# Performance work log

Hardware: AMD Instinct MI355X
Metric: run time of the kernel (lower is better)

## Reference

```python
import jax, jax.numpy as jnp
import numpy as np

NUM_LEVELS = 16
FEATS_PER_LEVEL = 2
LOG2_HASHMAP = 19
TABLE_SIZE = 1 << LOG2_HASHMAP
BASE_RES = 16
DESIRED_RES = 4096
PER_LEVEL_SCALE = float(np.exp(np.log(DESIRED_RES / BASE_RES) / (NUM_LEVELS - 1)))
PRIMES = (np.uint32(1), np.uint32(2654435761), np.uint32(805459861))
N_POINTS = 2_000_000


def _level_features(x, table, level):
    # x: [N,3] in [0,1]; table: [TABLE_SIZE, F]
    scale = BASE_RES * (PER_LEVEL_SCALE ** level) - 1.0
    res = int(np.ceil(scale)) + 1
    dense = (res ** 3) <= TABLE_SIZE  # tcnn uses dense indexing when grid fits
    pos = x * scale + 0.5
    pos0 = jnp.floor(pos)
    w = pos - pos0                     # trilinear weights, [N,3]
    base = pos0.astype(jnp.uint32)
    out = jnp.zeros((x.shape[0], table.shape[1]), dtype=table.dtype)
    for c in range(8):                 # 8 corners of the voxel
        offs = [(c >> d) & 1 for d in range(3)]
        pc = [jnp.minimum(base[:, d] + np.uint32(offs[d]), np.uint32(res - 1)) for d in range(3)]
        if dense:
            idx = pc[0] + pc[1] * np.uint32(res) + pc[2] * np.uint32(res * res)
        else:
            idx = (pc[0] * PRIMES[0]) ^ (pc[1] * PRIMES[1]) ^ (pc[2] * PRIMES[2])
            idx = idx & np.uint32(TABLE_SIZE - 1)
        wt = jnp.ones(x.shape[0], dtype=x.dtype)
        for d in range(3):
            wt = wt * (w[:, d] if offs[d] else (1.0 - w[:, d]))
        out = out + wt[:, None] * table[idx.astype(jnp.int32)]
    return out


def hashgrid_encode(x, tables):
    # x: [N,3] in [0,1]; tables: [L, TABLE_SIZE, F] -> [N, L*F]
    return jnp.concatenate(
        [_level_features(x, tables[l], l) for l in range(NUM_LEVELS)], axis=-1)


def setup_inputs() -> dict:
    key = jax.random.key(0)
    k1, k2, k3, k4, k5 = jax.random.split(key, 5)
    points = jax.random.uniform(k1, (N_POINTS, 3), dtype=jnp.float32)
    # tcnn hashgrid init: uniform(-1e-4, 1e-4)
    tables = jax.random.uniform(k2, (NUM_LEVELS, TABLE_SIZE, FEATS_PER_LEVEL),
                                minval=-1e-4, maxval=1e-4, dtype=jnp.float32)
    def kaiming(k, fan_out, fan_in):
        bound = np.sqrt(2.0) * np.sqrt(3.0 / fan_in)
        return jax.random.uniform(k, (fan_out, fan_in), minval=-bound, maxval=bound,
                                  dtype=jnp.float32)
    W1 = kaiming(k3, 32, 32)
    W2 = kaiming(k4, 32, 32)
    W3 = kaiming(k5, 4, 32)
    aabb = jnp.stack([jnp.zeros(3, jnp.float32), jnp.ones(3, jnp.float32)])
    return {"points": points, "tables": tables, "W1": W1, "W2": W2, "W3": W3,
            "aabb": aabb}


def reference(points, tables, W1, W2, W3, aabb):
    texc = jnp.clip((points - aabb[0][None, :]) / (aabb[1] - aabb[0])[None, :], 0.0, 1.0)
    enc = hashgrid_encode(texc, tables)            # [N, 32]
    h = jax.nn.relu(enc @ W1.T)
    h = jax.nn.relu(h @ W2.T)
    out = h @ W3.T                                 # [N, 4]
    mn = jnp.array([0.0, 0.0, 0.0, 0.01], dtype=out.dtype)
    mx = jnp.array([1.0, 1.0, 1.0, 1.0], dtype=out.dtype)
    return jax.nn.sigmoid(out) * (mx - mn) + mn
```

## Files before the change

kernel.cpp:

```cpp
#include <hip/hip_runtime.h>
#include <cmath>


namespace {
constexpr int kLevels = 16;
constexpr unsigned kTableSize = 1u << 19;
constexpr unsigned kMask = kTableSize - 1u;
constexpr int kCells = 262144;
constexpr int kScanBlocks = 256;

typedef _Float16 half2_t __attribute__((ext_vector_type(2)));
typedef unsigned int u32;

struct LevelParams {
  float scale[kLevels];
  unsigned res[kLevels];
  int dense[kLevels];
  unsigned toff[kLevels];
  unsigned cnt[kLevels];
};
}

__global__ __launch_bounds__(256)
void conv_tables_kernel(const float2* __restrict__ src, u32* __restrict__ dst,
                        LevelParams lp,
                        const float* __restrict__ W1, const float* __restrict__ W2,
                        const float* __restrict__ W3, half2_t* __restrict__ Wh,
                        u32* __restrict__ hist0)
{
  int gid = blockIdx.x * blockDim.x + threadIdx.x;
  if (gid < 512) {
    Wh[gid] = half2_t{(_Float16)W1[2 * gid], (_Float16)W1[2 * gid + 1]};
  } else if (gid < 1024) {
    int t = gid - 512;
    Wh[512 + t] = half2_t{(_Float16)W2[2 * t], (_Float16)W2[2 * t + 1]};
  } else if (gid < 1088) {
    int t = gid - 1024;
    Wh[1024 + t] = half2_t{(_Float16)W3[2 * t], (_Float16)W3[2 * t + 1]};
  }
  if (hist0 && gid < kCells) hist0[gid] = 0u;
  int l = blockIdx.x >> 11;
  unsigned e = (unsigned)((blockIdx.x & 2047) * blockDim.x + threadIdx.x);
  if (l < kLevels && e < lp.cnt[l]) {
    float2 v = src[(size_t)l * kTableSize + e];
    dst[lp.toff[l] + e] =
        __builtin_bit_cast(u32, half2_t{(_Float16)v.x, (_Float16)v.y});
  }
}

__device__ __forceinline__ void texc_of(const float* __restrict__ pts,
                                        const float* __restrict__ aabb, int i,
                                        float& x, float& y, float& z)
{
  float a0x = aabb[0], a0y = aabb[1], a0z = aabb[2];
  float a1x = aabb[3], a1y = aabb[4], a1z = aabb[5];
  x = fminf(fmaxf((pts[3 * i + 0] - a0x) / (a1x - a0x), 0.f), 1.f);
  y = fminf(fmaxf((pts[3 * i + 1] - a0y) / (a1y - a0y), 0.f), 1.f);
  z = fminf(fmaxf((pts[3 * i + 2] - a0z) / (a1z - a0z), 0.f), 1.f);
}

__device__ __forceinline__ int cell_of(float x, float y, float z)
{
  int cx = min((int)(x * 64.f), 63);
  int cy = min((int)(y * 64.f), 63);
  int cz = min((int)(z * 64.f), 63);
  return cx + (cy << 6) + (cz << 12);
}

__global__ __launch_bounds__(256)
void hist_kernel(const float* __restrict__ points, const float* __restrict__ aabb,
                 u32* __restrict__ hist, int n)
{
  int i = blockIdx.x * blockDim.x + threadIdx.x;
  if (i >= n) return;
  float x, y, z;
  texc_of(points, aabb, i, x, y, z);
  atomicAdd(&hist[cell_of(x, y, z)], 1u);
}

__global__ __launch_bounds__(1024)
void scanA_kernel(u32* __restrict__ hist, u32* __restrict__ btot)
{
  __shared__ u32 sm[1024];
  int t = threadIdx.x;
  int i = (blockIdx.x << 10) + t;
  u32 x = hist[i];
  sm[t] = x;
  __syncthreads();
  u32 v = x;
  for (int off = 1; off < 1024; off <<= 1) {
    u32 a = (t >= off) ? sm[t - off] : 0u;
    __syncthreads();
    v += a;
    sm[t] = v;
    __syncthreads();
  }
  hist[i] = v - x;
  if (t == 1023) btot[blockIdx.x] = v;
}

__global__ __launch_bounds__(256)
void scanB_kernel(const u32* __restrict__ btot, u32* __restrict__ bbase)
{
  __shared__ u32 sm[256];
  int t = threadIdx.x;
  u32 x = btot[t];
  sm[t] = x;
  __syncthreads();
  u32 v = x;
  for (int off = 1; off < 256; off <<= 1) {
    u32 a = (t >= off) ? sm[t - off] : 0u;
    __syncthreads();
    v += a;
    sm[t] = v;
    __syncthreads();
  }
  bbase[t] = v - x;
}

__global__ __launch_bounds__(256)
void scatter_kernel(const float* __restrict__ points, const float* __restrict__ aabb,
                    u32* __restrict__ hist, const u32* __restrict__ bbase,
                    float4* __restrict__ sorted, u32* __restrict__ perm, int n)
{
  int i = blockIdx.x * blockDim.x + threadIdx.x;
  if (i >= n) return;
  float x, y, z;
  texc_of(points, aabb, i, x, y, z);
  int c = cell_of(x, y, z);
  u32 slot = bbase[c >> 10] + atomicAdd(&hist[c], 1u);
  sorted[slot] = float4{x, y, z, 0.f};
  perm[slot] = (u32)i;
}

__device__ __forceinline__ u32 sel4(uint4 v, u32 j) {
  u32 lo = (j & 1u) ? v.y : v.x;
  u32 hi = (j & 1u) ? v.w : v.z;
  return (j & 2u) ? hi : lo;
}

__global__ __launch_bounds__(256)
void encode_kernel(const float4* __restrict__ pts,
                   const u32* __restrict__ tables,
                   half2_t* __restrict__ enc,
                   LevelParams lp, int n, int bpl)
{
  int l = blockIdx.x / bpl;
  int i = (blockIdx.x - l * bpl) * blockDim.x + threadIdx.x;
  if (i >= n) return;

  float4 p = pts[i];
  float x = p.x, y = p.y, z = p.z;

  float s = lp.scale[l];
  unsigned res = lp.res[l];
  bool dense = (lp.dense[l] != 0);
  unsigned rm1 = res - 1u;
  unsigned res2 = res * res;
  const u32* tab = tables + lp.toff[l];

  float fx = x * s + 0.5f, fy = y * s + 0.5f, fz = z * s + 0.5f;
  float fx0 = floorf(fx), fy0 = floorf(fy), fz0 = floorf(fz);
  float wx = fx - fx0, wy = fy - fy0, wz = fz - fz0;
  unsigned bx = (unsigned)fx0, by = (unsigned)fy0, bz = (unsigned)fz0;

  unsigned pcx0 = min(bx, rm1), pcx1 = min(bx + 1u, rm1);

  u32 idx0[4], idx1[4];
  #pragma unroll
  for (int q = 0; q < 4; ++q) {
    unsigned oy = (unsigned)(q & 1);
    unsigned oz = (unsigned)(q >> 1);
    unsigned pcy = min(by + oy, rm1);
    unsigned pcz = min(bz + oz, rm1);
    if (dense) {
      u32 b = pcy * res + pcz * res2;
      idx0[q] = pcx0 + b;
      idx1[q] = pcx1 + b;
    } else {
      u32 h = (pcy * 2654435761u) ^ (pcz * 805459861u);
      idx0[q] = (pcx0 ^ h) & kMask;
      idx1[q] = (pcx1 ^ h) & kMask;
    }
  }

  uint4 v[4];
  #pragma unroll
  for (int q = 0; q < 4; ++q)
    v[q] = *reinterpret_cast<const uint4*>(tab + (idx0[q] & ~3u));

  u32 e1x[4] = {0u, 0u, 0u, 0u};
  #pragma unroll
  for (int q = 0; q < 4; ++q) {
    if ((idx0[q] ^ idx1[q]) >= 4u) e1x[q] = tab[idx1[q]];
  }

  float wx1 = wx, wx0 = 1.f - wx;
  float acc0 = 0.f, acc1 = 0.f;
  #pragma unroll
  for (int q = 0; q < 4; ++q) {
    unsigned oy = (unsigned)(q & 1);
    unsigned oz = (unsigned)(q >> 1);
    float wyz = (oy ? wy : 1.f - wy) * (oz ? wz : 1.f - wz);
    u32 e0 = sel4(v[q], idx0[q] & 3u);
    u32 e1g = sel4(v[q], idx1[q] & 3u);
    u32 e1 = ((idx0[q] ^ idx1[q]) < 4u) ? e1g : e1x[q];
    half2_t f0 = __builtin_bit_cast(half2_t, e0);
    half2_t f1 = __builtin_bit_cast(half2_t, e1);
    float w0 = wyz * wx0, w1 = wyz * wx1;
    acc0 += w0 * (float)f0.x + w1 * (float)f1.x;
    acc1 += w0 * (float)f0.y + w1 * (float)f1.y;
  }
  enc[(size_t)l * n + i] = half2_t{(_Float16)acc0, (_Float16)acc1};
}

__global__ __launch_bounds__(256)
void encode_raw_kernel(const float* __restrict__ points,
                       const u32* __restrict__ tables,
                       const float* __restrict__ aabb,
                       half2_t* __restrict__ enc,
                       LevelParams lp, int n, int bpl)
{
  int l = blockIdx.x / bpl;
  int i = (blockIdx.x - l * bpl) * blockDim.x + threadIdx.x;
  if (i >= n) return;
  float x, y, z;
  texc_of(points, aabb, i, x, y, z);

  float s = lp.scale[l];
  unsigned res = lp.res[l];
  bool dense = (lp.dense[l] != 0);
  unsigned rm1 = res - 1u;
  unsigned res2 = res * res;
  const u32* tab = tables + lp.toff[l];

  float fx = x * s + 0.5f, fy = y * s + 0.5f, fz = z * s + 0.5f;
  float fx0 = floorf(fx), fy0 = floorf(fy), fz0 = floorf(fz);
  float wx = fx - fx0, wy = fy - fy0, wz = fz - fz0;
  unsigned bx = (unsigned)fx0, by = (unsigned)fy0, bz = (unsigned)fz0;
  unsigned pcx0 = min(bx, rm1), pcx1 = min(bx + 1u, rm1);

  u32 idx0[4], idx1[4];
  #pragma unroll
  for (int q = 0; q < 4; ++q) {
    unsigned oy = (unsigned)(q & 1);
    unsigned oz = (unsigned)(q >> 1);
    unsigned pcy = min(by + oy, rm1);
    unsigned pcz = min(bz + oz, rm1);
    if (dense) {
      u32 b = pcy * res + pcz * res2;
      idx0[q] = pcx0 + b;
      idx1[q] = pcx1 + b;
    } else {
      u32 h = (pcy * 2654435761u) ^ (pcz * 805459861u);
      idx0[q] = (pcx0 ^ h) & kMask;
      idx1[q] = (pcx1 ^ h) & kMask;
    }
  }
  uint4 v[4];
  #pragma unroll
  for (int q = 0; q < 4; ++q)
    v[q] = *reinterpret_cast<const uint4*>(tab + (idx0[q] & ~3u));
  u32 e1x[4] = {0u, 0u, 0u, 0u};
  #pragma unroll
  for (int q = 0; q < 4; ++q) {
    if ((idx0[q] ^ idx1[q]) >= 4u) e1x[q] = tab[idx1[q]];
  }
  float wx1 = wx, wx0 = 1.f - wx;
  float acc0 = 0.f, acc1 = 0.f;
  #pragma unroll
  for (int q = 0; q < 4; ++q) {
    unsigned oy = (unsigned)(q & 1);
    unsigned oz = (unsigned)(q >> 1);
    float wyz = (oy ? wy : 1.f - wy) * (oz ? wz : 1.f - wz);
    u32 e0 = sel4(v[q], idx0[q] & 3u);
    u32 e1g = sel4(v[q], idx1[q] & 3u);
    u32 e1 = ((idx0[q] ^ idx1[q]) < 4u) ? e1g : e1x[q];
    half2_t f0 = __builtin_bit_cast(half2_t, e0);
    half2_t f1 = __builtin_bit_cast(half2_t, e1);
    float w0 = wyz * wx0, w1 = wyz * wx1;
    acc0 += w0 * (float)f0.x + w1 * (float)f1.x;
    acc1 += w0 * (float)f0.y + w1 * (float)f1.y;
  }
  enc[(size_t)l * n + i] = half2_t{(_Float16)acc0, (_Float16)acc1};
}

__device__ __forceinline__ float dot2_acc(half2_t a, half2_t b, float c) {
#if __has_builtin(__builtin_amdgcn_fdot2)
  return __builtin_amdgcn_fdot2(a, b, c, false);
#else
  return c + (float)a.x * (float)b.x + (float)a.y * (float)b.y;
#endif
}

__global__ __launch_bounds__(256)
void mlp_kernel(const half2_t* __restrict__ enc,
                const half2_t* __restrict__ Wh,
                const u32* __restrict__ perm,
                float* __restrict__ out, int n)
{
  int i = blockIdx.x * blockDim.x + threadIdx.x;
  if (i >= n) return;

  u32 orig = perm ? perm[i] : (u32)i;

  half2_t e[16];
  #pragma unroll
  for (int l = 0; l < kLevels; ++l) e[l] = enc[(size_t)l * n + i];

  const half2_t* W1h = Wh;
  const half2_t* W2h = Wh + 512;
  const half2_t* W3h = Wh + 1024;

  float h1f[32];
  #pragma unroll
  for (int j = 0; j < 32; ++j) {
    float acc = 0.f;
    #pragma unroll
    for (int k = 0; k < 16; ++k) acc = dot2_acc(e[k], W1h[16 * j + k], acc);
    h1f[j] = fmaxf(acc, 0.f);
  }
  half2_t h1[16];
  #pragma unroll
  for (int k = 0; k < 16; ++k)
    h1[k] = half2_t{(_Float16)h1f[2 * k], (_Float16)h1f[2 * k + 1]};

  float h2f[32];
  #pragma unroll
  for (int j = 0; j < 32; ++j) {
    float acc = 0.f;
    #pragma unroll
    for (int k = 0; k < 16; ++k) acc = dot2_acc(h1[k], W2h[16 * j + k], acc);
    h2f[j] = fmaxf(acc, 0.f);
  }
  half2_t h2[16];
  #pragma unroll
  for (int k = 0; k < 16; ++k)
    h2[k] = half2_t{(_Float16)h2f[2 * k], (_Float16)h2f[2 * k + 1]};

  float o[4];
  #pragma unroll
  for (int j = 0; j < 4; ++j) {
    float acc = 0.f;
    #pragma unroll
    for (int k = 0; k < 16; ++k) acc = dot2_acc(h2[k], W3h[16 * j + k], acc);
    o[j] = acc;
  }

  float4 r;
  r.x = 1.f / (1.f + __expf(-o[0]));
  r.y = 1.f / (1.f + __expf(-o[1]));
  r.z = 1.f / (1.f + __expf(-o[2]));
  r.w = 0.99f / (1.f + __expf(-o[3])) + 0.01f;
  reinterpret_cast<float4*>(out)[orig] = r;
}

__global__ __launch_bounds__(256)
void hashgrid_mlp_kernel(const float* __restrict__ points,
                         const float* __restrict__ tables,
                         const float* __restrict__ W1,
                         const float* __restrict__ W2,
                         const float* __restrict__ W3,
                         const float* __restrict__ aabb,
                         float* __restrict__ out,
                         LevelParams lp, int n)
{
  int i = blockIdx.x * blockDim.x + threadIdx.x;
  if (i >= n) return;
  float x, y, z;
  texc_of(points, aabb, i, x, y, z);
  float enc[2 * kLevels];
  #pragma unroll
  for (int l = 0; l < kLevels; ++l) {
    float s = lp.scale[l];
    unsigned res = lp.res[l];
    bool dense = (lp.dense[l] != 0);
    unsigned rm1 = res - 1u;
    unsigned res2 = res * res;
    float fx = x * s + 0.5f, fy = y * s + 0.5f, fz = z * s + 0.5f;
    float fx0 = floorf(fx), fy0 = floorf(fy), fz0 = floorf(fz);
    float wx = fx - fx0, wy = fy - fy0, wz = fz - fz0;
    unsigned bx = (unsigned)fx0, by = (unsigned)fy0, bz = (unsigned)fz0;
    const float2* tab = reinterpret_cast<const float2*>(tables) + (size_t)l * kTableSize;
    float acc0 = 0.f, acc1 = 0.f;
    #pragma unroll
    for (int c = 0; c < 8; ++c) {
      unsigned ox = (unsigned)(c & 1);
      unsigned oy = (unsigned)((c >> 1) & 1);
      unsigned oz = (unsigned)((c >> 2) & 1);
      unsigned pcx = min(bx + ox, rm1);
      unsigned pcy = min(by + oy, rm1);
      unsigned pcz = min(bz + oz, rm1);
      unsigned idx;
      if (dense) idx = pcx + pcy * res + pcz * res2;
      else idx = (pcx ^ (pcy * 2654435761u) ^ (pcz * 805459861u)) & kMask;
      float wt = (ox ? wx : 1.f - wx) * (oy ? wy : 1.f - wy) * (oz ? wz : 1.f - wz);
      float2 f = tab[idx];
      acc0 += wt * f.x;
      acc1 += wt * f.y;
    }
    enc[2 * l + 0] = acc0;
    enc[2 * l + 1] = acc1;
  }
  float h1[32];
  #pragma unroll
  for (int j = 0; j < 32; ++j) {
    float acc = 0.f;
    #pragma unroll
    for (int k = 0; k < 32; ++k) acc += enc[k] * W1[32 * j + k];
    h1[j] = fmaxf(acc, 0.f);
  }
  float h2[32];
  #pragma unroll
  for (int j = 0; j < 32; ++j) {
    float acc = 0.f;
    #pragma unroll
    for (int k = 0; k < 32; ++k) acc += h1[k] * W2[32 * j + k];
    h2[j] = fmaxf(acc, 0.f);
  }
  float o[4];
  #pragma unroll
  for (int j = 0; j < 4; ++j) {
    float acc = 0.f;
    #pragma unroll
    for (int k = 0; k < 32; ++k) acc += h2[k] * W3[32 * j + k];
    o[j] = acc;
  }
  float4 r;
  r.x = 1.f / (1.f + __expf(-o[0]));
  r.y = 1.f / (1.f + __expf(-o[1]));
  r.z = 1.f / (1.f + __expf(-o[2]));
  r.w = 0.99f / (1.f + __expf(-o[3])) + 0.01f;
  reinterpret_cast<float4*>(out)[i] = r;
}

extern "C" void kernel_launch(void* const* d_in, const int* in_sizes, int n_in,
                              void* d_out, int out_size, void* d_ws, size_t ws_size,
                              hipStream_t stream) {
  const float* points = (const float*)d_in[0];
  const float* tables = (const float*)d_in[1];
  const float* W1     = (const float*)d_in[2];
  const float* W2     = (const float*)d_in[3];
  const float* W3     = (const float*)d_in[4];
  const float* aabb   = (const float*)d_in[5];
  float* out = (float*)d_out;
  int n = in_sizes[0] / 3;

  LevelParams lp;
  const double pls = std::exp(std::log(4096.0 / 16.0) / 15.0);
  unsigned off = 0;
  for (int l = 0; l < kLevels; ++l) {
    double s = 16.0 * std::pow(pls, (double)l) - 1.0;
    lp.scale[l] = (float)s;
    long long res = (long long)std::ceil(s) + 1;
    lp.res[l] = (unsigned)res;
    long long r3 = res * res * res;
    lp.dense[l] = (r3 <= (long long)kTableSize) ? 1 : 0;
    lp.cnt[l] = lp.dense[l] ? (unsigned)r3 : kTableSize;
    lp.toff[l] = off;
    off += (lp.cnt[l] + 3u) & ~3u;
  }

  const int block = 256;
  const size_t tab_f16_bytes = (size_t)off * sizeof(u32);
  const size_t enc_bytes     = (size_t)kLevels * (size_t)n * sizeof(half2_t);
  const size_t perm_bytes    = (size_t)n * sizeof(u32);
  const size_t w_bytes       = 1088 * sizeof(half2_t);

  const size_t need_sorted = tab_f16_bytes + enc_bytes + perm_bytes + w_bytes;
  const size_t need_raw    = tab_f16_bytes + enc_bytes + w_bytes;
  const bool out_fits_sorted = (size_t)out_size >= (size_t)4 * (size_t)n;
  const bool enc_fits_hist = enc_bytes >= (size_t)(kCells + 512) * sizeof(u32);

  const int grid_n = (n + block - 1) / block;
  const int bpl = grid_n;

  if (ws_size >= need_sorted && out_fits_sorted && enc_fits_hist) {
    char* p = (char*)d_ws;
    u32*     tab_f16 = (u32*)p;                   p += tab_f16_bytes;
    half2_t* enc     = (half2_t*)p;               p += enc_bytes;
    u32*     perm    = (u32*)p;                   p += perm_bytes;
    half2_t* Wh      = (half2_t*)p;
    u32*     hist    = (u32*)enc;
    u32*     btot    = hist + kCells;
    u32*     bbase   = btot + kScanBlocks;
    float4*  sorted  = (float4*)d_out;

    conv_tables_kernel<<<kLevels * 2048, block, 0, stream>>>(
        reinterpret_cast<const float2*>(tables), tab_f16, lp, W1, W2, W3, Wh, hist);
    hist_kernel<<<grid_n, block, 0, stream>>>(points, aabb, hist, n);
    scanA_kernel<<<kScanBlocks, 1024, 0, stream>>>(hist, btot);
    scanB_kernel<<<1, 256, 0, stream>>>(btot, bbase);
    scatter_kernel<<<grid_n, block, 0, stream>>>(points, aabb, hist, bbase,
                                                 sorted, perm, n);
    encode_kernel<<<bpl * kLevels, block, 0, stream>>>(
        sorted, tab_f16, enc, lp, n, bpl);
    mlp_kernel<<<grid_n, block, 0, stream>>>(enc, Wh, perm, out, n);
  } else if (ws_size >= need_raw) {
    char* p = (char*)d_ws;
    u32*     tab_f16 = (u32*)p;                   p += tab_f16_bytes;
    half2_t* enc     = (half2_t*)p;               p += enc_bytes;
    half2_t* Wh      = (half2_t*)p;

    conv_tables_kernel<<<kLevels * 2048, block, 0, stream>>>(
        reinterpret_cast<const float2*>(tables), tab_f16, lp, W1, W2, W3, Wh,
        nullptr);
    encode_raw_kernel<<<bpl * kLevels, block, 0, stream>>>(
        points, tab_f16, aabb, enc, lp, n, bpl);
    mlp_kernel<<<grid_n, block, 0, stream>>>(enc, Wh, nullptr, out, n);
  } else {
    hashgrid_mlp_kernel<<<grid_n, block, 0, stream>>>(
        points, tables, W1, W2, W3, aabb, out, lp, n);
  }
}
```

Baseline: 799.7 us.

## Fuse per-level encode and MLP into one kernel on sorted points

Replaces the separate level-parallel encode kernel and MLP kernel on the sorted path with a single kernel that computes all 16 levels per point and runs the MLP in registers. This removes the intermediate fp16 encoding buffer write and read. The sorted points, perm and histogram now live in workspace instead of aliasing the output and encoding buffers. In exchange, each thread keeps all level lookups and MLP state in registers, so register pressure rises and occupancy may drop. Table locality also changes, since levels are no longer processed one at a time across the grid.

```diff
diff --git a/kernel.cpp b/kernel.cpp
--- a/kernel.cpp
+++ b/kernel.cpp
@@ -139,18 +139,152 @@
   return (j & 2u) ? hi : lo;
 }
 
-__global__ __launch_bounds__(256)
-void encode_kernel(const float4* __restrict__ pts,
-                   const u32* __restrict__ tables,
-                   half2_t* __restrict__ enc,
-                   LevelParams lp, int n, int bpl)
+__device__ __forceinline__ float dot2_acc(half2_t a, half2_t b, float c) {
+#if __has_builtin(__builtin_amdgcn_fdot2)
+  return __builtin_amdgcn_fdot2(a, b, c, false);
+#else
+  return c + (float)a.x * (float)b.x + (float)a.y * (float)b.y;
+#endif
+}
+
+__global__ __launch_bounds__(256)
+void fused_kernel(const float4* __restrict__ pts,
+                  const u32* __restrict__ tables,
+                  const half2_t* __restrict__ Wh,
+                  const u32* __restrict__ perm,
+                  float* __restrict__ out,
+                  LevelParams lp, int n)
+{
+  int i = blockIdx.x * blockDim.x + threadIdx.x;
+  if (i >= n) return;
+
+  u32 orig = perm[i];
+  float4 p = pts[i];
+  float x = p.x, y = p.y, z = p.z;
+
+  half2_t e[kLevels];
+  #pragma unroll
+  for (int l = 0; l < kLevels; ++l) {
+    float s = lp.scale[l];
+    unsigned res = lp.res[l];
+    bool dense = (lp.dense[l] != 0);
+    unsigned rm1 = res - 1u;
+    unsigned res2 = res * res;
+    const u32* tab = tables + lp.toff[l];
+
+    float fx = x * s + 0.5f, fy = y * s + 0.5f, fz = z * s + 0.5f;
+    float fx0 = floorf(fx), fy0 = floorf(fy), fz0 = floorf(fz);
+    float wx = fx - fx0, wy = fy - fy0, wz = fz - fz0;
+    unsigned bx = (unsigned)fx0, by = (unsigned)fy0, bz = (unsigned)fz0;
+    unsigned pcx0 = min(bx, rm1), pcx1 = min(bx + 1u, rm1);
+
+    u32 idx0[4], idx1[4];
+    #pragma unroll
+    for (int q = 0; q < 4; ++q) {
+      unsigned oy = (unsigned)(q & 1);
+      unsigned oz = (unsigned)(q >> 1);
+      unsigned pcy = min(by + oy, rm1);
+      unsigned pcz = min(bz + oz, rm1);
+      if (dense) {
+        u32 b = pcy * res + pcz * res2;
+        idx0[q] = pcx0 + b;
+        idx1[q] = pcx1 + b;
+      } else {
+        u32 h = (pcy * 2654435761u) ^ (pcz * 805459861u);
+        idx0[q] = (pcx0 ^ h) & kMask;
+        idx1[q] = (pcx1 ^ h) & kMask;
+      }
+    }
+
+    uint4 v[4];
+    #pragma unroll
+    for (int q = 0; q < 4; ++q)
+      v[q] = *reinterpret_cast<const uint4*>(tab + (idx0[q] & ~3u));
+
+    u32 e1x[4] = {0u, 0u, 0u, 0u};
+    #pragma unroll
+    for (int q = 0; q < 4; ++q) {
+      if ((idx0[q] ^ idx1[q]) >= 4u) e1x[q] = tab[idx1[q]];
+    }
+
+    float wx1 = wx, wx0 = 1.f - wx;
+    float acc0 = 0.f, acc1 = 0.f;
+    #pragma unroll
+    for (int q = 0; q < 4; ++q) {
+      unsigned oy = (unsigned)(q & 1);
+      unsigned oz = (unsigned)(q >> 1);
+      float wyz = (oy ? wy : 1.f - wy) * (oz ? wz : 1.f - wz);
+      u32 e0 = sel4(v[q], idx0[q] & 3u);
+      u32 e1g = sel4(v[q], idx1[q] & 3u);
+      u32 e1 = ((idx0[q] ^ idx1[q]) < 4u) ? e1g : e1x[q];
+      half2_t f0 = __builtin_bit_cast(half2_t, e0);
+      half2_t f1 = __builtin_bit_cast(half2_t, e1);
+      float w0 = wyz * wx0, w1 = wyz * wx1;
+      acc0 += w0 * (float)f0.x + w1 * (float)f1.x;
+      acc1 += w0 * (float)f0.y + w1 * (float)f1.y;
+    }
+    e[l] = half2_t{(_Float16)acc0, (_Float16)acc1};
+  }
+
+  const half2_t* W1h = Wh;
+  const half2_t* W2h = Wh + 512;
+  const half2_t* W3h = Wh + 1024;
+
+  float h1f[32];
+  #pragma unroll
+  for (int j = 0; j < 32; ++j) {
+    float acc = 0.f;
+    #pragma unroll
+    for (int k = 0; k < 16; ++k) acc = dot2_acc(e[k], W1h[16 * j + k], acc);
+    h1f[j] = fmaxf(acc, 0.f);
+  }
+  half2_t h1[16];
+  #pragma unroll
+  for (int k = 0; k < 16; ++k)
+    h1[k] = half2_t{(_Float16)h1f[2 * k], (_Float16)h1f[2 * k + 1]};
+
+  float h2f[32];
+  #pragma unroll
+  for (int j = 0; j < 32; ++j) {
+    float acc = 0.f;
+    #pragma unroll
+    for (int k = 0; k < 16; ++k) acc = dot2_acc(h1[k], W2h[16 * j + k], acc);
+    h2f[j] = fmaxf(acc, 0.f);
+  }
+  half2_t h2[16];
+  #pragma unroll
+  for (int k = 0; k < 16; ++k)
+    h2[k] = half2_t{(_Float16)h2f[2 * k], (_Float16)h2f[2 * k + 1]};
+
+  float o[4];
+  #pragma unroll
+  for (int j = 0; j < 4; ++j) {
+    float acc = 0.f;
+    #pragma unroll
+    for (int k = 0; k < 16; ++k) acc = dot2_acc(h2[k], W3h[16 * j + k], acc);
+    o[j] = acc;
+  }
+
+  float4 r;
+  r.x = 1.f / (1.f + __expf(-o[0]));
+  r.y = 1.f / (1.f + __expf(-o[1]));
+  r.z = 1.f / (1.f + __expf(-o[2]));
+  r.w = 0.99f / (1.f + __expf(-o[3])) + 0.01f;
+  reinterpret_cast<float4*>(out)[orig] = r;
+}
+
+__global__ __launch_bounds__(256)
+void encode_raw_kernel(const float* __restrict__ points,
+                       const u32* __restrict__ tables,
+                       const float* __restrict__ aabb,
+                       half2_t* __restrict__ enc,
+                       LevelParams lp, int n, int bpl)
 {
   int l = blockIdx.x / bpl;
   int i = (blockIdx.x - l * bpl) * blockDim.x + threadIdx.x;
   if (i >= n) return;
-
-  float4 p = pts[i];
-  float x = p.x, y = p.y, z = p.z;
+  float x, y, z;
+  texc_of(points, aabb, i, x, y, z);
 
   float s = lp.scale[l];
   unsigned res = lp.res[l];
@@ -163,7 +297,6 @@
   float fx0 = floorf(fx), fy0 = floorf(fy), fz0 = floorf(fz);
   float wx = fx - fx0, wy = fy - fy0, wz = fz - fz0;
   unsigned bx = (unsigned)fx0, by = (unsigned)fy0, bz = (unsigned)fz0;
-
   unsigned pcx0 = min(bx, rm1), pcx1 = min(bx + 1u, rm1);
 
   u32 idx0[4], idx1[4];
@@ -183,18 +316,15 @@
       idx1[q] = (pcx1 ^ h) & kMask;
     }
   }
-
   uint4 v[4];
   #pragma unroll
   for (int q = 0; q < 4; ++q)
     v[q] = *reinterpret_cast<const uint4*>(tab + (idx0[q] & ~3u));
-
   u32 e1x[4] = {0u, 0u, 0u, 0u};
   #pragma unroll
   for (int q = 0; q < 4; ++q) {
     if ((idx0[q] ^ idx1[q]) >= 4u) e1x[q] = tab[idx1[q]];
   }
-
   float wx1 = wx, wx0 = 1.f - wx;
   float acc0 = 0.f, acc1 = 0.f;
   #pragma unroll
@@ -215,94 +345,12 @@
 }
 
 __global__ __launch_bounds__(256)
-void encode_raw_kernel(const float* __restrict__ points,
-                       const u32* __restrict__ tables,
-                       const float* __restrict__ aabb,
-                       half2_t* __restrict__ enc,
-                       LevelParams lp, int n, int bpl)
-{
-  int l = blockIdx.x / bpl;
-  int i = (blockIdx.x - l * bpl) * blockDim.x + threadIdx.x;
-  if (i >= n) return;
-  float x, y, z;
-  texc_of(points, aabb, i, x, y, z);
-
-  float s = lp.scale[l];
-  unsigned res = lp.res[l];
-  bool dense = (lp.dense[l] != 0);
-  unsigned rm1 = res - 1u;
-  unsigned res2 = res * res;
-  const u32* tab = tables + lp.toff[l];
-
-  float fx = x * s + 0.5f, fy = y * s + 0.5f, fz = z * s + 0.5f;
-  float fx0 = floorf(fx), fy0 = floorf(fy), fz0 = floorf(fz);
-  float wx = fx - fx0, wy = fy - fy0, wz = fz - fz0;
-  unsigned bx = (unsigned)fx0, by = (unsigned)fy0, bz = (unsigned)fz0;
-  unsigned pcx0 = min(bx, rm1), pcx1 = min(bx + 1u, rm1);
-
-  u32 idx0[4], idx1[4];
-  #pragma unroll
-  for (int q = 0; q < 4; ++q) {
-    unsigned oy = (unsigned)(q & 1);
-    unsigned oz = (unsigned)(q >> 1);
-    unsigned pcy = min(by + oy, rm1);
-    unsigned pcz = min(bz + oz, rm1);
-    if (dense) {
-      u32 b = pcy * res + pcz * res2;
-      idx0[q] = pcx0 + b;
-      idx1[q] = pcx1 + b;
-    } else {
-      u32 h = (pcy * 2654435761u) ^ (pcz * 805459861u);
-      idx0[q] = (pcx0 ^ h) & kMask;
-      idx1[q] = (pcx1 ^ h) & kMask;
-    }
-  }
-  uint4 v[4];
-  #pragma unroll
-  for (int q = 0; q < 4; ++q)
-    v[q] = *reinterpret_cast<const uint4*>(tab + (idx0[q] & ~3u));
-  u32 e1x[4] = {0u, 0u, 0u, 0u};
-  #pragma unroll
-  for (int q = 0; q < 4; ++q) {
-    if ((idx0[q] ^ idx1[q]) >= 4u) e1x[q] = tab[idx1[q]];
-  }
-  float wx1 = wx, wx0 = 1.f - wx;
-  float acc0 = 0.f, acc1 = 0.f;
-  #pragma unroll
-  for (int q = 0; q < 4; ++q) {
-    unsigned oy = (unsigned)(q & 1);
-    unsigned oz = (unsigned)(q >> 1);
-    float wyz = (oy ? wy : 1.f - wy) * (oz ? wz : 1.f - wz);
-    u32 e0 = sel4(v[q], idx0[q] & 3u);
-    u32 e1g = sel4(v[q], idx1[q] & 3u);
-    u32 e1 = ((idx0[q] ^ idx1[q]) < 4u) ? e1g : e1x[q];
-    half2_t f0 = __builtin_bit_cast(half2_t, e0);
-    half2_t f1 = __builtin_bit_cast(half2_t, e1);
-    float w0 = wyz * wx0, w1 = wyz * wx1;
-    acc0 += w0 * (float)f0.x + w1 * (float)f1.x;
-    acc1 += w0 * (float)f0.y + w1 * (float)f1.y;
-  }
-  enc[(size_t)l * n + i] = half2_t{(_Float16)acc0, (_Float16)acc1};
-}
-
-__device__ __forceinline__ float dot2_acc(half2_t a, half2_t b, float c) {
-#if __has_builtin(__builtin_amdgcn_fdot2)
-  return __builtin_amdgcn_fdot2(a, b, c, false);
-#else
-  return c + (float)a.x * (float)b.x + (float)a.y * (float)b.y;
-#endif
-}
-
-__global__ __launch_bounds__(256)
 void mlp_kernel(const half2_t* __restrict__ enc,
                 const half2_t* __restrict__ Wh,
-                const u32* __restrict__ perm,
                 float* __restrict__ out, int n)
 {
   int i = blockIdx.x * blockDim.x + threadIdx.x;
   if (i >= n) return;
-
-  u32 orig = perm ? perm[i] : (u32)i;
 
   half2_t e[16];
   #pragma unroll
@@ -352,7 +400,7 @@
   r.y = 1.f / (1.f + __expf(-o[1]));
   r.z = 1.f / (1.f + __expf(-o[2]));
   r.w = 0.99f / (1.f + __expf(-o[3])) + 0.01f;
-  reinterpret_cast<float4*>(out)[orig] = r;
+  reinterpret_cast<float4*>(out)[i] = r;
 }
 
 __global__ __launch_bounds__(256)
@@ -463,28 +511,26 @@
 
   const int block = 256;
   const size_t tab_f16_bytes = (size_t)off * sizeof(u32);
+  const size_t sorted_bytes  = (size_t)n * sizeof(float4);
+  const size_t perm_bytes    = (size_t)n * sizeof(u32);
+  const size_t hist_bytes    = (size_t)(kCells + 2 * kScanBlocks) * sizeof(u32);
   const size_t enc_bytes     = (size_t)kLevels * (size_t)n * sizeof(half2_t);
-  const size_t perm_bytes    = (size_t)n * sizeof(u32);
   const size_t w_bytes       = 1088 * sizeof(half2_t);
 
-  const size_t need_sorted = tab_f16_bytes + enc_bytes + perm_bytes + w_bytes;
+  const size_t need_sorted = tab_f16_bytes + sorted_bytes + perm_bytes + hist_bytes + w_bytes;
   const size_t need_raw    = tab_f16_bytes + enc_bytes + w_bytes;
-  const bool out_fits_sorted = (size_t)out_size >= (size_t)4 * (size_t)n;
-  const bool enc_fits_hist = enc_bytes >= (size_t)(kCells + 512) * sizeof(u32);
 
   const int grid_n = (n + block - 1) / block;
-  const int bpl = grid_n;
-
-  if (ws_size >= need_sorted && out_fits_sorted && enc_fits_hist) {
+
+  if (ws_size >= need_sorted) {
     char* p = (char*)d_ws;
     u32*     tab_f16 = (u32*)p;                   p += tab_f16_bytes;
-    half2_t* enc     = (half2_t*)p;               p += enc_bytes;
+    float4*  sorted  = (float4*)p;                p += sorted_bytes;
     u32*     perm    = (u32*)p;                   p += perm_bytes;
+    u32*     hist    = (u32*)p;                   p += hist_bytes;
     half2_t* Wh      = (half2_t*)p;
-    u32*     hist    = (u32*)enc;
     u32*     btot    = hist + kCells;
     u32*     bbase   = btot + kScanBlocks;
-    float4*  sorted  = (float4*)d_out;
 
     conv_tables_kernel<<<kLevels * 2048, block, 0, stream>>>(
         reinterpret_cast<const float2*>(tables), tab_f16, lp, W1, W2, W3, Wh, hist);
@@ -493,21 +539,21 @@
     scanB_kernel<<<1, 256, 0, stream>>>(btot, bbase);
     scatter_kernel<<<grid_n, block, 0, stream>>>(points, aabb, hist, bbase,
                                                  sorted, perm, n);
-    encode_kernel<<<bpl * kLevels, block, 0, stream>>>(
-        sorted, tab_f16, enc, lp, n, bpl);
-    mlp_kernel<<<grid_n, block, 0, stream>>>(enc, Wh, perm, out, n);
+    fused_kernel<<<grid_n, block, 0, stream>>>(sorted, tab_f16, Wh, perm, out,
+                                               lp, n);
   } else if (ws_size >= need_raw) {
     char* p = (char*)d_ws;
     u32*     tab_f16 = (u32*)p;                   p += tab_f16_bytes;
     half2_t* enc     = (half2_t*)p;               p += enc_bytes;
     half2_t* Wh      = (half2_t*)p;
 
+    const int bpl = grid_n;
     conv_tables_kernel<<<kLevels * 2048, block, 0, stream>>>(
         reinterpret_cast<const float2*>(tables), tab_f16, lp, W1, W2, W3, Wh,
         nullptr);
     encode_raw_kernel<<<bpl * kLevels, block, 0, stream>>>(
         points, tab_f16, aabb, enc, lp, n, bpl);
-    mlp_kernel<<<grid_n, block, 0, stream>>>(enc, Wh, nullptr, out, n);
+    mlp_kernel<<<grid_n, block, 0, stream>>>(enc, Wh, out, n);
   } else {
     hashgrid_mlp_kernel<<<grid_n, block, 0, stream>>>(
         points, tables, W1, W2, W3, aabb, out, lp, n);
```

Result: slower. 1.495 ms (+87.0%).

## Morton-order cell sort, fold scanB into scatter, pack perm into sorted points

Applied to the files above, without the earlier changes.

Replaces linear cell indexing with a Morton (Z-order) code so sorted points have better 3D locality for table gathers. Removes the separate single-block scan kernel by having each scatter block redo the 256-entry block-total scan in shared memory. Stores the original index in the w lane of the sorted float4, dropping the perm buffer, and the MLP reads it back from there. The sorted buffer moves from the output buffer into workspace, which adds redundant per-block scan work in exchange for one fewer launch. The MLP loops are also restructured to compute two outputs at a time directly in half precision.

```diff
diff --git a/kernel.cpp b/kernel.cpp
--- a/kernel.cpp
+++ b/kernel.cpp
@@ -59,12 +59,22 @@
   z = fminf(fmaxf((pts[3 * i + 2] - a0z) / (a1z - a0z), 0.f), 1.f);
 }
 
-__device__ __forceinline__ int cell_of(float x, float y, float z)
-{
-  int cx = min((int)(x * 64.f), 63);
-  int cy = min((int)(y * 64.f), 63);
-  int cz = min((int)(z * 64.f), 63);
-  return cx + (cy << 6) + (cz << 12);
+__device__ __forceinline__ u32 expand3(u32 v)
+{
+  v &= 0x3FFu;
+  v = (v | (v << 16)) & 0x030000FFu;
+  v = (v | (v << 8))  & 0x0300F00Fu;
+  v = (v | (v << 4))  & 0x030C30C3u;
+  v = (v | (v << 2))  & 0x09249249u;
+  return v;
+}
+
+__device__ __forceinline__ u32 cell_of(float x, float y, float z)
+{
+  u32 cx = (u32)min((int)(x * 64.f), 63);
+  u32 cy = (u32)min((int)(y * 64.f), 63);
+  u32 cz = (u32)min((int)(z * 64.f), 63);
+  return expand3(cx) | (expand3(cy) << 1) | (expand3(cz) << 2);
 }
 
 __global__ __launch_bounds__(256)
@@ -100,43 +110,49 @@
 }
 
 __global__ __launch_bounds__(256)
-void scanB_kernel(const u32* __restrict__ btot, u32* __restrict__ bbase)
-{
-  __shared__ u32 sm[256];
+void scatter_kernel(const float* __restrict__ points, const float* __restrict__ aabb,
+                    u32* __restrict__ hist, const u32* __restrict__ btot,
+                    float4* __restrict__ sorted, int n)
+{
+  __shared__ u32 bb[kScanBlocks];
   int t = threadIdx.x;
-  u32 x = btot[t];
-  sm[t] = x;
+  u32 xv = btot[t];
+  bb[t] = xv;
   __syncthreads();
-  u32 v = x;
+  u32 v = xv;
   for (int off = 1; off < 256; off <<= 1) {
-    u32 a = (t >= off) ? sm[t - off] : 0u;
+    u32 a = (t >= off) ? bb[t - off] : 0u;
     __syncthreads();
     v += a;
-    sm[t] = v;
+    bb[t] = v;
     __syncthreads();
   }
-  bbase[t] = v - x;
-}
-
-__global__ __launch_bounds__(256)
-void scatter_kernel(const float* __restrict__ points, const float* __restrict__ aabb,
-                    u32* __restrict__ hist, const u32* __restrict__ bbase,
-                    float4* __restrict__ sorted, u32* __restrict__ perm, int n)
-{
-  int i = blockIdx.x * blockDim.x + threadIdx.x;
+  u32 excl = v - xv;
+  __syncthreads();
+  bb[t] = excl;
+  __syncthreads();
+
+  int i = blockIdx.x * 256 + t;
   if (i >= n) return;
   float x, y, z;
   texc_of(points, aabb, i, x, y, z);
-  int c = cell_of(x, y, z);
-  u32 slot = bbase[c >> 10] + atomicAdd(&hist[c], 1u);
-  sorted[slot] = float4{x, y, z, 0.f};
-  perm[slot] = (u32)i;
+  u32 c = cell_of(x, y, z);
+  u32 slot = bb[c >> 10] + atomicAdd(&hist[c], 1u);
+  sorted[slot] = float4{x, y, z, __builtin_bit_cast(float, (u32)i)};
 }
 
 __device__ __forceinline__ u32 sel4(uint4 v, u32 j) {
   u32 lo = (j & 1u) ? v.y : v.x;
   u32 hi = (j & 1u) ? v.w : v.z;
   return (j & 2u) ? hi : lo;
+}
+
+__device__ __forceinline__ float dot2_acc(half2_t a, half2_t b, float c) {
+#if __has_builtin(__builtin_amdgcn_fdot2)
+  return __builtin_amdgcn_fdot2(a, b, c, false);
+#else
+  return c + (float)a.x * (float)b.x + (float)a.y * (float)b.y;
+#endif
 }
 
 __global__ __launch_bounds__(256)
@@ -285,24 +301,16 @@
   enc[(size_t)l * n + i] = half2_t{(_Float16)acc0, (_Float16)acc1};
 }
 
-__device__ __forceinline__ float dot2_acc(half2_t a, half2_t b, float c) {
-#if __has_builtin(__builtin_amdgcn_fdot2)
-  return __builtin_amdgcn_fdot2(a, b, c, false);
-#else
-  return c + (float)a.x * (float)b.x + (float)a.y * (float)b.y;
-#endif
-}
-
 __global__ __launch_bounds__(256)
 void mlp_kernel(const half2_t* __restrict__ enc,
                 const half2_t* __restrict__ Wh,
-                const u32* __restrict__ perm,
+                const float* __restrict__ sortedw,
                 float* __restrict__ out, int n)
 {
   int i = blockIdx.x * blockDim.x + threadIdx.x;
   if (i >= n) return;
 
-  u32 orig = perm ? perm[i] : (u32)i;
+  u32 orig = sortedw ? __builtin_bit_cast(u32, sortedw[4 * i + 3]) : (u32)i;
 
   half2_t e[16];
   #pragma unroll
@@ -312,31 +320,29 @@
   const half2_t* W2h = Wh + 512;
   const half2_t* W3h = Wh + 1024;
 
-  float h1f[32];
-  #pragma unroll
-  for (int j = 0; j < 32; ++j) {
-    float acc = 0.f;
-    #pragma unroll
-    for (int k = 0; k < 16; ++k) acc = dot2_acc(e[k], W1h[16 * j + k], acc);
-    h1f[j] = fmaxf(acc, 0.f);
-  }
   half2_t h1[16];
   #pragma unroll
-  for (int k = 0; k < 16; ++k)
-    h1[k] = half2_t{(_Float16)h1f[2 * k], (_Float16)h1f[2 * k + 1]};
-
-  float h2f[32];
-  #pragma unroll
-  for (int j = 0; j < 32; ++j) {
-    float acc = 0.f;
-    #pragma unroll
-    for (int k = 0; k < 16; ++k) acc = dot2_acc(h1[k], W2h[16 * j + k], acc);
-    h2f[j] = fmaxf(acc, 0.f);
-  }
+  for (int jj = 0; jj < 16; ++jj) {
+    float a0 = 0.f, a1 = 0.f;
+    #pragma unroll
+    for (int k = 0; k < 16; ++k) {
+      a0 = dot2_acc(e[k], W1h[16 * (2 * jj) + k], a0);
+      a1 = dot2_acc(e[k], W1h[16 * (2 * jj + 1) + k], a1);
+    }
+    h1[jj] = half2_t{(_Float16)fmaxf(a0, 0.f), (_Float16)fmaxf(a1, 0.f)};
+  }
+
   half2_t h2[16];
   #pragma unroll
-  for (int k = 0; k < 16; ++k)
-    h2[k] = half2_t{(_Float16)h2f[2 * k], (_Float16)h2f[2 * k + 1]};
+  for (int jj = 0; jj < 16; ++jj) {
+    float a0 = 0.f, a1 = 0.f;
+    #pragma unroll
+    for (int k = 0; k < 16; ++k) {
+      a0 = dot2_acc(h1[k], W2h[16 * (2 * jj) + k], a0);
+      a1 = dot2_acc(h1[k], W2h[16 * (2 * jj + 1) + k], a1);
+    }
+    h2[jj] = half2_t{(_Float16)fmaxf(a0, 0.f), (_Float16)fmaxf(a1, 0.f)};
+  }
 
   float o[4];
   #pragma unroll
@@ -463,39 +469,60 @@
 
   const int block = 256;
   const size_t tab_f16_bytes = (size_t)off * sizeof(u32);
+  const size_t sorted_bytes  = (size_t)n * sizeof(float4);
+  const size_t hist_bytes    = (size_t)(kCells + kScanBlocks) * sizeof(u32);
   const size_t enc_bytes     = (size_t)kLevels * (size_t)n * sizeof(half2_t);
-  const size_t perm_bytes    = (size_t)n * sizeof(u32);
   const size_t w_bytes       = 1088 * sizeof(half2_t);
 
-  const size_t need_sorted = tab_f16_bytes + enc_bytes + perm_bytes + w_bytes;
-  const size_t need_raw    = tab_f16_bytes + enc_bytes + w_bytes;
-  const bool out_fits_sorted = (size_t)out_size >= (size_t)4 * (size_t)n;
-  const bool enc_fits_hist = enc_bytes >= (size_t)(kCells + 512) * sizeof(u32);
+  const size_t need_sorted = tab_f16_bytes + sorted_bytes + hist_bytes +
+                             enc_bytes + w_bytes;
+  const size_t need_sorted_real = tab_f16_bytes + sorted_bytes + enc_bytes + w_bytes;
+  const size_t need_sorted_tight = tab_f16_bytes + enc_bytes + w_bytes +
+                                   ((size_t)n * sizeof(u32));
+  (void)need_sorted_tight;
+
+  const size_t need_raw = tab_f16_bytes + enc_bytes + w_bytes;
+  const bool out_fits_scratch = (size_t)out_size >= (size_t)4 * (size_t)n;
 
   const int grid_n = (n + block - 1) / block;
   const int bpl = grid_n;
 
-  if (ws_size >= need_sorted && out_fits_sorted && enc_fits_hist) {
+  if (ws_size >= need_sorted_real) {
     char* p = (char*)d_ws;
     u32*     tab_f16 = (u32*)p;                   p += tab_f16_bytes;
+    float4*  sorted  = (float4*)p;                p += sorted_bytes;
     half2_t* enc     = (half2_t*)p;               p += enc_bytes;
-    u32*     perm    = (u32*)p;                   p += perm_bytes;
     half2_t* Wh      = (half2_t*)p;
     u32*     hist    = (u32*)enc;
     u32*     btot    = hist + kCells;
-    u32*     bbase   = btot + kScanBlocks;
-    float4*  sorted  = (float4*)d_out;
 
     conv_tables_kernel<<<kLevels * 2048, block, 0, stream>>>(
         reinterpret_cast<const float2*>(tables), tab_f16, lp, W1, W2, W3, Wh, hist);
     hist_kernel<<<grid_n, block, 0, stream>>>(points, aabb, hist, n);
     scanA_kernel<<<kScanBlocks, 1024, 0, stream>>>(hist, btot);
-    scanB_kernel<<<1, 256, 0, stream>>>(btot, bbase);
-    scatter_kernel<<<grid_n, block, 0, stream>>>(points, aabb, hist, bbase,
-                                                 sorted, perm, n);
+    scatter_kernel<<<grid_n, block, 0, stream>>>(points, aabb, hist, btot,
+                                                 sorted, n);
     encode_kernel<<<bpl * kLevels, block, 0, stream>>>(
         sorted, tab_f16, enc, lp, n, bpl);
-    mlp_kernel<<<grid_n, block, 0, stream>>>(enc, Wh, perm, out, n);
+    mlp_kernel<<<grid_n, block, 0, stream>>>(enc, Wh, (const float*)sorted, out, n);
+  } else if (ws_size >= need_raw && out_fits_scratch) {
+    char* p = (char*)d_ws;
+    u32*     tab_f16 = (u32*)p;                   p += tab_f16_bytes;
+    half2_t* enc     = (half2_t*)p;               p += enc_bytes;
+    half2_t* Wh      = (half2_t*)p;
+    u32*     hist    = (u32*)enc;
+    u32*     btot    = hist + kCells;
+    float4*  sorted  = (float4*)d_out;
+
+    conv_tables_kernel<<<kLevels * 2048, block, 0, stream>>>(
+        reinterpret_cast<const float2*>(tables), tab_f16, lp, W1, W2, W3, Wh, hist);
+    hist_kernel<<<grid_n, block, 0, stream>>>(points, aabb, hist, n);
+    scanA_kernel<<<kScanBlocks, 1024, 0, stream>>>(hist, btot);
+    scatter_kernel<<<grid_n, block, 0, stream>>>(points, aabb, hist, btot,
+                                                 sorted, n);
+    encode_kernel<<<bpl * kLevels, block, 0, stream>>>(
+        sorted, tab_f16, enc, lp, n, bpl);
+    mlp_kernel<<<grid_n, block, 0, stream>>>(enc, Wh, (const float*)sorted, out, n);
   } else if (ws_size >= need_raw) {
     char* p = (char*)d_ws;
     u32*     tab_f16 = (u32*)p;                   p += tab_f16_bytes;
```

Result: slower. 821.2 us (+2.7%).
